# Performance work log

Measured on AMD Instinct MI355X. Metric: run time of the kernel, lower is better.

The kernel has to match this reference:

```python
import jax, jax.numpy as jnp
import numpy as np

L, S, B, E, H, FF = 2048, 2048, 4, 1024, 16, 4096
HD = E // H
EPS = 1e-5


def _ln(x, g, b):
    mu = jnp.mean(x, axis=-1, keepdims=True)
    var = jnp.mean(jnp.square(x - mu), axis=-1, keepdims=True)
    return (x - mu) * jax.lax.rsqrt(var + EPS) * g + b


def _mha(xq, xk, xv, Wq, bq, Wk, bk, Wv, bv, Wo, bo, mask):
    l, bsz, e = xq.shape
    s = xk.shape[0]
    q = (xq @ Wq.T + bq).reshape(l, bsz, H, HD)
    k = (xk @ Wk.T + bk).reshape(s, bsz, H, HD)
    v = (xv @ Wv.T + bv).reshape(s, bsz, H, HD)
    scores = jnp.einsum('lbhd,sbhd->bhls', q, k) / (float(HD) ** 0.5)
    if mask is not None:
        scores = scores + mask  # broadcast (L,S) over (B,H,L,S)
    w = jax.nn.softmax(scores, axis=-1)
    out = jnp.einsum('bhls,sbhd->lbhd', w, v).reshape(l, bsz, e)
    return out @ Wo.T + bo


def setup_inputs() -> dict:
    key = jax.random.key(0)
    ks = jax.random.split(key, 32)
    sc = 0.02
    d = {
        'tgt': jax.random.normal(ks[0], (L, B, E), jnp.float32),
        'memory': jax.random.normal(ks[1], (S, B, E), jnp.float32),
        'tgt_mask': jnp.where(jnp.triu(jnp.ones((L, L), bool), k=1), -jnp.inf, 0.0).astype(jnp.float32),
    }
    def lin(i, out_d, in_d):
        return jax.random.normal(ks[i], (out_d, in_d), jnp.float32) * sc, jnp.zeros((out_d,), jnp.float32)
    for pfx, base in (('sa', 2), ('ca', 6)):
        for j, nm in enumerate(('Wq', 'Wk', 'Wv', 'Wo')):
            W, b = lin(base + j, E, E)
            d[f'{pfx}_{nm}'] = W
            d[f'{pfx}_b{nm[1]}'] = b
    d['W1'], d['b1'] = lin(10, FF, E)
    d['W2'], d['b2'] = lin(11, E, FF)
    for i, nm in enumerate(('ln1', 'ln2', 'ln3')):
        d[f'{nm}_g'] = jnp.ones((E,), jnp.float32)
        d[f'{nm}_b'] = jnp.zeros((E,), jnp.float32)
    return d


def reference(tgt, memory, tgt_mask,
              sa_Wq, sa_bq, sa_Wk, sa_bk, sa_Wv, sa_bv, sa_Wo, sa_bo,
              ca_Wq, ca_bq, ca_Wk, ca_bk, ca_Wv, ca_bv, ca_Wo, ca_bo,
              W1, b1, W2, b2,
              ln1_g, ln1_b, ln2_g, ln2_b, ln3_g, ln3_b):
    # masked self-attention + residual + norm1
    sa = _mha(tgt, tgt, tgt, sa_Wq, sa_bq, sa_Wk, sa_bk, sa_Wv, sa_bv, sa_Wo, sa_bo, tgt_mask)
    x = _ln(tgt + sa, ln1_g, ln1_b)
    # cross-attention + residual + norm2
    ca = _mha(x, memory, memory, ca_Wq, ca_bq, ca_Wk, ca_bk, ca_Wv, ca_bv, ca_Wo, ca_bo, None)
    x = _ln(x + ca, ln2_g, ln2_b)
    # FFN + residual + norm3 (dropout = identity in eval)
    ffn = jax.nn.relu(x @ W1.T + b1) @ W2.T + b2
    return _ln(x + ffn, ln3_g, ln3_b)
```

## Files before the change

kernel.cpp:

```cpp
#include <hip/hip_runtime.h>
#include <cstdint>

typedef unsigned short u16;
typedef __bf16 bf16x8 __attribute__((ext_vector_type(8)));
typedef float f32x4 __attribute__((ext_vector_type(4)));

#define L_ 2048
#define S_ 2048
#define B_ 4
#define E_ 1024
#define H_ 16
#define FF_ 4096
#define M_ (L_*B_)

#define QK_SCALE 0.18033688f

__device__ __forceinline__ unsigned f2bf(float f) {
  unsigned u = __float_as_uint(f);
  return (u + 0x7fffu + ((u >> 16) & 1u)) >> 16;
}
__device__ __forceinline__ float bflo(unsigned u){ return __uint_as_float(u << 16); }
__device__ __forceinline__ float bfhi(unsigned u){ return __uint_as_float(u & 0xffff0000u); }

struct CvtSeg { const float* src; u16* dst; int blk_end; };
struct CvtTab { CvtSeg s[6]; };

__global__ __launch_bounds__(256) void cvt_all(CvtTab t, int nseg) {
  const int blk = blockIdx.x;
  int k = 0;
  while (k < nseg - 1 && blk >= t.s[k].blk_end) k++;
  const int b0 = (k == 0) ? 0 : t.s[k-1].blk_end;
  const int off = (blk - b0) * 1024 + threadIdx.x * 4;
  float4 f = *(const float4*)(t.s[k].src + off);
  uint2 u;
  u.x = f2bf(f.x) | (f2bf(f.y) << 16);
  u.y = f2bf(f.z) | (f2bf(f.w) << 16);
  *(uint2*)(t.s[k].dst + off) = u;
}

struct GTab { u16* o[3]; const float* b[3]; float sc[3]; };

__device__ __forceinline__ void gl_lds16(const u16* g, u16* l) {
  __builtin_amdgcn_global_load_lds(
      (const __attribute__((address_space(1))) unsigned int*)g,
      (__attribute__((address_space(3))) unsigned int*)l, 16, 0, 0);
}

#define RAW_BARRIER() do { \
  asm volatile("" ::: "memory"); \
  __builtin_amdgcn_s_barrier(); \
  asm volatile("" ::: "memory"); \
} while (0)

template<int RELU, int NG>
__global__ __launch_bounds__(512, 2) void gemm256(
    const u16* __restrict__ A,
    const u16* __restrict__ Bw,
    GTab t, int K, int N)
{
  extern __shared__ __align__(16) u16 LDs[];
  const int tid  = threadIdx.x;
  const int lane = tid & 63;
  const int quad = lane >> 4;
  const int l16  = lane & 15;
  const int w    = tid >> 6;
  const int wm   = w >> 2;
  const int wn   = w & 3;
  const int bm = blockIdx.y << 8;
  const int bn = blockIdx.x << 8;

  const int grp = (NG > 1) ? ((int)blockIdx.x >> 2) : 0;
  u16* Cb = t.o[grp];
  const float* bias = t.b[grp];
  const float scale = t.sc[grp];
  const int ld = (NG > 1) ? 1024 : N;

  const int srow = (w << 4) + (lane >> 2);
  const int cg8  = ((lane & 3) ^ ((lane >> 3) & 3)) << 3;
  const u16* pa0 = A  + (size_t)(bm + srow) * K + cg8;
  const u16* pa1 = pa0 + (size_t)128 * K;
  const u16* pb0 = Bw + (size_t)(bn + srow) * K + cg8;
  const u16* pb1 = pb0 + (size_t)128 * K;
  const int wds = w << 9;

  const int swz  = (quad ^ ((l16 >> 1) & 3)) << 3;
  const int aoff = ((wm << 7) + l16) * 32 + swz;
  const int boff = 8192 + ((wn << 6) + l16) * 32 + swz;

  f32x4 acc[8][4];
  #pragma unroll
  for (int i = 0; i < 8; i++)
    #pragma unroll
    for (int j = 0; j < 4; j++)
      acc[i][j] = (f32x4){0.f, 0.f, 0.f, 0.f};

  const int nk = K >> 5;

  #pragma unroll
  for (int kt = 0; kt < 3; kt++) {
    const int sb = kt << 14;
    gl_lds16(pa0 + kt*32, LDs + sb + wds);
    gl_lds16(pa1 + kt*32, LDs + sb + 4096  + wds);
    gl_lds16(pb0 + kt*32, LDs + sb + 8192  + wds);
    gl_lds16(pb1 + kt*32, LDs + sb + 12288 + wds);
  }
  pa0 += 96; pa1 += 96; pb0 += 96; pb1 += 96;
  asm volatile("s_waitcnt vmcnt(8)" ::: "memory");
  RAW_BARRIER();

  for (int it = 0; it < nk; ++it) {
    const int rb = (it & 3) << 14;
    const int sb = ((it + 3) & 3) << 14;

    bf16x8 bfr[4], afr[4];
    #pragma unroll
    for (int nt = 0; nt < 4; nt++)
      bfr[nt] = *(const bf16x8*)(LDs + rb + boff + nt*512);
    #pragma unroll
    for (int mt = 0; mt < 4; mt++)
      afr[mt] = *(const bf16x8*)(LDs + rb + aoff + mt*512);
    gl_lds16(pa0, LDs + sb + wds);
    gl_lds16(pa1, LDs + sb + 4096 + wds);
    RAW_BARRIER();
    __builtin_amdgcn_s_setprio(1);
    #pragma unroll
    for (int mt = 0; mt < 4; mt++)
      #pragma unroll
      for (int nt = 0; nt < 4; nt++)
        acc[mt][nt] = __builtin_amdgcn_mfma_f32_16x16x32_bf16(afr[mt], bfr[nt], acc[mt][nt], 0, 0, 0);
    __builtin_amdgcn_s_setprio(0);
    RAW_BARRIER();

    #pragma unroll
    for (int mt = 0; mt < 4; mt++)
      afr[mt] = *(const bf16x8*)(LDs + rb + aoff + (4 + mt)*512);
    gl_lds16(pb0, LDs + sb + 8192  + wds);
    gl_lds16(pb1, LDs + sb + 12288 + wds);
    asm volatile("s_waitcnt vmcnt(8)" ::: "memory");
    RAW_BARRIER();
    __builtin_amdgcn_s_setprio(1);
    #pragma unroll
    for (int mt = 0; mt < 4; mt++)
      #pragma unroll
      for (int nt = 0; nt < 4; nt++)
        acc[4 + mt][nt] = __builtin_amdgcn_mfma_f32_16x16x32_bf16(afr[mt], bfr[nt], acc[4 + mt][nt], 0, 0, 0);
    __builtin_amdgcn_s_setprio(0);
    RAW_BARRIER();

    if (it + 4 < nk) { pa0 += 32; pa1 += 32; pb0 += 32; pb1 += 32; }
  }

  #pragma unroll
  for (int nt = 0; nt < 4; nt++) {
    const int col = bn + (wn << 6) + nt*16 + l16;
    const int ocol = (NG > 1) ? (col & 1023) : col;
    const float bv = bias[ocol];
    #pragma unroll
    for (int mt = 0; mt < 8; mt++) {
      #pragma unroll
      for (int i = 0; i < 4; i++) {
        const int row = bm + (wm << 7) + mt*16 + quad*4 + i;
        float v = (acc[mt][nt][i] + bv) * scale;
        if (RELU) v = fmaxf(v, 0.0f);
        Cb[(size_t)row * ld + ocol] = (u16)f2bf(v);
      }
    }
  }
}

template<int RELU>
__global__ __launch_bounds__(512, 2) void gemm256n(
    const u16* __restrict__ A,
    const u16* __restrict__ Bw,
    const float* __restrict__ bias,
    u16* __restrict__ C,
    float scale, int K, int N)
{
  extern __shared__ __align__(16) u16 LDs[];
  const int tid  = threadIdx.x;
  const int lane = tid & 63;
  const int quad = lane >> 4;
  const int l16  = lane & 15;
  const int w    = tid >> 6;
  const int wm   = w >> 1;
  const int wn   = w & 1;
  const int bm = blockIdx.y << 8;
  const int bn = blockIdx.x << 7;

  const int srow = (w << 4) + (lane >> 2);
  const int cg8  = ((lane & 3) ^ ((lane >> 3) & 3)) << 3;
  const u16* pa0 = A  + (size_t)(bm + srow) * K + cg8;
  const u16* pa1 = pa0 + (size_t)128 * K;
  const u16* pb0 = Bw + (size_t)(bn + srow) * K + cg8;
  const int wds = w << 9;

  const int swz  = (quad ^ ((l16 >> 1) & 3)) << 3;
  const int aoff = ((wm << 6) + l16) * 32 + swz;
  const int boff = 8192 + ((wn << 6) + l16) * 32 + swz;

  f32x4 acc[4][4];
  #pragma unroll
  for (int i = 0; i < 4; i++)
    #pragma unroll
    for (int j = 0; j < 4; j++)
      acc[i][j] = (f32x4){0.f, 0.f, 0.f, 0.f};

  const int nk = K >> 5;

  #pragma unroll
  for (int kt = 0; kt < 2; kt++) {
    const int sb = kt * 12288;
    gl_lds16(pa0 + kt*32, LDs + sb + wds);
    gl_lds16(pa1 + kt*32, LDs + sb + 4096 + wds);
    gl_lds16(pb0 + kt*32, LDs + sb + 8192 + wds);
  }
  pa0 += 64; pa1 += 64; pb0 += 64;
  asm volatile("s_waitcnt vmcnt(3)" ::: "memory");
  RAW_BARRIER();

  int rb = 0, sb = 24576;
  for (int it = 0; it < nk; ++it) {
    bf16x8 bfr[4], afr0, afr1;
    #pragma unroll
    for (int nt = 0; nt < 4; nt++)
      bfr[nt] = *(const bf16x8*)(LDs + rb + boff + nt*512);
    afr0 = *(const bf16x8*)(LDs + rb + aoff);
    afr1 = *(const bf16x8*)(LDs + rb + aoff + 512);
    gl_lds16(pa0, LDs + sb + wds);
    gl_lds16(pa1, LDs + sb + 4096 + wds);
    RAW_BARRIER();
    __builtin_amdgcn_s_setprio(1);
    #pragma unroll
    for (int nt = 0; nt < 4; nt++) {
      acc[0][nt] = __builtin_amdgcn_mfma_f32_16x16x32_bf16(afr0, bfr[nt], acc[0][nt], 0, 0, 0);
      acc[1][nt] = __builtin_amdgcn_mfma_f32_16x16x32_bf16(afr1, bfr[nt], acc[1][nt], 0, 0, 0);
    }
    __builtin_amdgcn_s_setprio(0);
    RAW_BARRIER();

    afr0 = *(const bf16x8*)(LDs + rb + aoff + 1024);
    afr1 = *(const bf16x8*)(LDs + rb + aoff + 1536);
    gl_lds16(pb0, LDs + sb + 8192 + wds);
    asm volatile("s_waitcnt vmcnt(3)" ::: "memory");
    RAW_BARRIER();
    __builtin_amdgcn_s_setprio(1);
    #pragma unroll
    for (int nt = 0; nt < 4; nt++) {
      acc[2][nt] = __builtin_amdgcn_mfma_f32_16x16x32_bf16(afr0, bfr[nt], acc[2][nt], 0, 0, 0);
      acc[3][nt] = __builtin_amdgcn_mfma_f32_16x16x32_bf16(afr1, bfr[nt], acc[3][nt], 0, 0, 0);
    }
    __builtin_amdgcn_s_setprio(0);
    RAW_BARRIER();

    if (it + 3 < nk) { pa0 += 32; pa1 += 32; pb0 += 32; }
    rb += 12288; if (rb == 36864) rb = 0;
    sb += 12288; if (sb == 36864) sb = 0;
  }

  #pragma unroll
  for (int nt = 0; nt < 4; nt++) {
    const int col = bn + (wn << 6) + nt*16 + l16;
    const float bv = bias[col];
    #pragma unroll
    for (int mt = 0; mt < 4; mt++) {
      #pragma unroll
      for (int i = 0; i < 4; i++) {
        const int row = bm + (wm << 6) + mt*16 + quad*4 + i;
        float v = (acc[mt][nt][i] + bv) * scale;
        if (RELU) v = fmaxf(v, 0.0f);
        C[(size_t)row * N + col] = (u16)f2bf(v);
      }
    }
  }
}

__global__ __launch_bounds__(256) void transpose_v(
    const u16* __restrict__ V, u16* __restrict__ Vt)
{
  const int t = threadIdx.x;
  const int lane = t & 63;
  const int w = t >> 6;
  const int bh = blockIdx.y;
  const int b = bh >> 4, h = bh & 15;
  const int l = (blockIdx.x << 6) + lane;
  const size_t vrow = ((size_t)l * B_ + b) * E_ + h * 64;
  #pragma unroll
  for (int g = 0; g < 2; g++) {
    const int d0 = w * 8 + g * 32;
    uint4 u = *(const uint4*)(V + vrow + d0);
    u16 e[8];
    e[0] = u.x & 0xffff; e[1] = u.x >> 16;
    e[2] = u.y & 0xffff; e[3] = u.y >> 16;
    e[4] = u.z & 0xffff; e[5] = u.z >> 16;
    e[6] = u.w & 0xffff; e[7] = u.w >> 16;
    #pragma unroll
    for (int j = 0; j < 8; j++)
      Vt[(size_t)(bh * 64 + d0 + j) * S_ + l] = e[j];
  }
}

template<int CAUSAL>
__global__ __launch_bounds__(256, 4) void attn_mfma(
    const u16* __restrict__ Q,
    const u16* __restrict__ Kg,
    const u16* __restrict__ Vt,
    u16* __restrict__ O,
    int Skv)
{
  __shared__ __align__(16) u16 Tile[16384];
  const int tid  = threadIdx.x;
  const int lane = tid & 63;
  const int w    = tid >> 6;
  const int l16  = lane & 15;
  const int quad = lane >> 4;
  const int bh = blockIdx.x;
  const int b = bh >> 4, h = bh & 15;
  const int y = blockIdx.y;
  const int q0 = (CAUSAL ? ((y < 8) ? (15 - 2*y) : (2*y - 16)) : y) << 7;
  const int wq = q0 + w*32;

  bf16x8 qf[2][2];
  #pragma unroll
  for (int h2 = 0; h2 < 2; h2++) {
    const size_t qoff = ((size_t)(wq + h2*16 + l16) * B_ + b) * E_ + h*64;
    qf[h2][0] = *(const bf16x8*)(Q + qoff + quad*8);
    qf[h2][1] = *(const bf16x8*)(Q + qoff + 32 + quad*8);
  }

  f32x4 oacc[2][4];
  #pragma unroll
  for (int h2 = 0; h2 < 2; h2++)
    #pragma unroll
    for (int i = 0; i < 4; i++) oacc[h2][i] = (f32x4){0.f,0.f,0.f,0.f};
  float lsum[2] = {0.f, 0.f};

  const int lrow = lane >> 3;
  const int lchunk = (lane & 7) ^ lrow;
  const u16* kp = Kg + ((size_t)(16*w + lrow) * B_ + b) * E_ + h*64 + lchunk*8;
  const u16* vp = Vt + (size_t)(bh*64 + 16*w + lrow) * Skv + lchunk*8;
  const size_t kRow8 = (size_t)8 * B_ * E_;
  const size_t kTile = (size_t)64 * B_ * E_;
  u16* ldsK = Tile + w*1024;
  u16* ldsV = Tile + 4096 + w*1024;

  const int pbase = 8192 + w*2048;
  int aKV[2], aW[4];
  #pragma unroll
  for (int kh = 0; kh < 2; kh++)
    aKV[kh] = l16*64 + (((kh*4 + quad) ^ (l16 & 7)) << 3);
  #pragma unroll
  for (int st = 0; st < 4; st++)
    aW[st] = pbase + l16*64 +
             ((((st*2) + (quad >> 1)) ^ (l16 & 7)) << 3) + ((quad & 1) << 2);

  const int send = CAUSAL ? (q0 + 128) : Skv;
  for (int s0 = 0; s0 < send; s0 += 64) {
    __syncthreads();
    gl_lds16(kp,         ldsK);
    gl_lds16(kp + kRow8, ldsK + 512);
    gl_lds16(vp,         ldsV);
    gl_lds16(vp + 8*Skv, ldsV + 512);
    kp += kTile; vp += 64;
    __syncthreads();

    if (CAUSAL && s0 >= wq + 32) continue;

    f32x4 sacc[2][4];
    #pragma unroll
    for (int h2 = 0; h2 < 2; h2++)
      #pragma unroll
      for (int st = 0; st < 4; st++) sacc[h2][st] = (f32x4){0.f,0.f,0.f,0.f};
    #pragma unroll
    for (int kh = 0; kh < 2; kh++)
      #pragma unroll
      for (int st = 0; st < 4; st++) {
        bf16x8 kf = *(const bf16x8*)(Tile + aKV[kh] + st*1024);
        sacc[0][st] = __builtin_amdgcn_mfma_f32_16x16x32_bf16(kf, qf[0][kh], sacc[0][st], 0, 0, 0);
        sacc[1][st] = __builtin_amdgcn_mfma_f32_16x16x32_bf16(kf, qf[1][kh], sacc[1][st], 0, 0, 0);
      }

    #pragma unroll
    for (int h2 = 0; h2 < 2; h2++) {
      float p[16];
      #pragma unroll
      for (int st = 0; st < 4; st++)
        #pragma unroll
        for (int r = 0; r < 4; r++) p[st*4+r] = sacc[h2][st][r];
      if (CAUSAL && s0 + 63 > wq + h2*16) {
        const int qa = wq + h2*16 + l16;
        #pragma unroll
        for (int st = 0; st < 4; st++)
          #pragma unroll
          for (int r = 0; r < 4; r++)
            if (s0 + st*16 + quad*4 + r > qa) p[st*4+r] = -3e38f;
      }
      #pragma unroll
      for (int i = 0; i < 16; i++) p[i] = exp2f(p[i]);
      float s01 = (p[0]+p[1]) + (p[2]+p[3]);
      float s23 = (p[4]+p[5]) + (p[6]+p[7]);
      float s45 = (p[8]+p[9]) + (p[10]+p[11]);
      float s67 = (p[12]+p[13]) + (p[14]+p[15]);
      lsum[h2] += (s01+s23) + (s45+s67);

      #pragma unroll
      for (int st = 0; st < 4; st++) {
        uint2 d;
        d.x = __builtin_amdgcn_perm(__float_as_uint(p[st*4+1]), __float_as_uint(p[st*4+0]), 0x07060302u);
        d.y = __builtin_amdgcn_perm(__float_as_uint(p[st*4+3]), __float_as_uint(p[st*4+2]), 0x07060302u);
        *(uint2*)(Tile + aW[st] + h2*1024) = d;
      }
    }

    #pragma unroll
    for (int kh = 0; kh < 2; kh++) {
      bf16x8 pf[2];
      #pragma unroll
      for (int h2 = 0; h2 < 2; h2++)
        pf[h2] = *(const bf16x8*)(Tile + pbase + h2*1024 + aKV[kh]);
      #pragma unroll
      for (int dt = 0; dt < 4; dt++) {
        bf16x8 vf = *(const bf16x8*)(Tile + 4096 + aKV[kh] + dt*1024);
        #pragma unroll
        for (int h2 = 0; h2 < 2; h2++)
          oacc[h2][dt] = __builtin_amdgcn_mfma_f32_16x16x32_bf16(pf[h2], vf, oacc[h2][dt], 0, 0, 0);
      }
    }
  }

  #pragma unroll
  for (int h2 = 0; h2 < 2; h2++) {
    float rs = lsum[h2];
    rs += __shfl_xor(rs, 16);
    rs += __shfl_xor(rs, 32);
    const float inv = 1.0f / rs;
    #pragma unroll
    for (int r = 0; r < 4; r++) {
      const float li = __shfl(inv, (quad << 2) + r);
      const int qg = wq + h2*16 + quad*4 + r;
      const size_t orow = ((size_t)qg * B_ + b) * E_ + h*64;
      #pragma unroll
      for (int dt = 0; dt < 4; dt++)
        O[orow + dt*16 + l16] = (u16)f2bf(oacc[h2][dt][r] * li);
    }
  }
}

template<int RF32>
__global__ __launch_bounds__(256) void add_ln(
    const u16* __restrict__ X,
    const float* __restrict__ Rf, const u16* __restrict__ Rb,
    const float* __restrict__ g, const float* __restrict__ be,
    float* __restrict__ outF, u16* __restrict__ outB)
{
  const int row = blockIdx.x;
  const int tid = threadIdx.x;
  const size_t base = (size_t)row * E_;
  uint2 xu = *(const uint2*)(X + base + tid*4);
  float x0 = bflo(xu.x), x1 = bfhi(xu.x), x2 = bflo(xu.y), x3 = bfhi(xu.y);
  float r0, r1, r2, r3;
  if (RF32) {
    float4 rv = *(const float4*)(Rf + base + tid*4);
    r0 = rv.x; r1 = rv.y; r2 = rv.z; r3 = rv.w;
  } else {
    uint2 ru = *(const uint2*)(Rb + base + tid*4);
    r0 = bflo(ru.x); r1 = bfhi(ru.x); r2 = bflo(ru.y); r3 = bfhi(ru.y);
  }
  const float v0 = x0 + r0, v1 = x1 + r1, v2 = x2 + r2, v3 = x3 + r3;
  float s  = v0 + v1 + v2 + v3;
  float s2 = v0*v0 + v1*v1 + v2*v2 + v3*v3;
  #pragma unroll
  for (int off = 32; off >= 1; off >>= 1) {
    s  += __shfl_down(s,  off);
    s2 += __shfl_down(s2, off);
  }
  __shared__ float ps[4], ps2[4];
  const int wv = tid >> 6, lane = tid & 63;
  if (lane == 0) { ps[wv] = s; ps2[wv] = s2; }
  __syncthreads();
  const float ts  = ps[0] + ps[1] + ps[2] + ps[3];
  const float ts2 = ps2[0] + ps2[1] + ps2[2] + ps2[3];
  const float mu  = ts * (1.0f / E_);
  const float var = ts2 * (1.0f / E_) - mu * mu;
  const float rsq = rsqrtf(var + 1e-5f);
  float4 gv = *(const float4*)(g  + tid*4);
  float4 bv = *(const float4*)(be + tid*4);
  const float o0 = (v0 - mu) * rsq * gv.x + bv.x;
  const float o1 = (v1 - mu) * rsq * gv.y + bv.y;
  const float o2 = (v2 - mu) * rsq * gv.z + bv.z;
  const float o3 = (v3 - mu) * rsq * gv.w + bv.w;
  if (outF) {
    float4 ov; ov.x = o0; ov.y = o1; ov.z = o2; ov.w = o3;
    *(float4*)(outF + base + tid*4) = ov;
  }
  if (outB) {
    uint2 u;
    u.x = f2bf(o0) | (f2bf(o1) << 16);
    u.y = f2bf(o2) | (f2bf(o3) << 16);
    *(uint2*)(outB + base + tid*4) = u;
  }
}

extern "C" void kernel_launch(void* const* d_in, const int* in_sizes, int n_in,
                              void* d_out, int out_size, void* d_ws, size_t ws_size,
                              hipStream_t stream) {
  (void)in_sizes; (void)n_in; (void)out_size; (void)ws_size;
  const float* tgt  = (const float*)d_in[0];
  const float* mem  = (const float*)d_in[1];
  const float* saWq = (const float*)d_in[3];  const float* sabq = (const float*)d_in[4];
  const float* saWk = (const float*)d_in[5];  const float* sabk = (const float*)d_in[6];
  const float* saWv = (const float*)d_in[7];  const float* sabv = (const float*)d_in[8];
  const float* saWo = (const float*)d_in[9];  const float* sabo = (const float*)d_in[10];
  const float* caWq = (const float*)d_in[11]; const float* cabq = (const float*)d_in[12];
  const float* caWk = (const float*)d_in[13]; const float* cabk = (const float*)d_in[14];
  const float* caWv = (const float*)d_in[15]; const float* cabv = (const float*)d_in[16];
  const float* caWo = (const float*)d_in[17]; const float* cabo = (const float*)d_in[18];
  const float* W1   = (const float*)d_in[19]; const float* b1   = (const float*)d_in[20];
  const float* W2   = (const float*)d_in[21]; const float* b2   = (const float*)d_in[22];
  const float* ln1g = (const float*)d_in[23]; const float* ln1b = (const float*)d_in[24];
  const float* ln2g = (const float*)d_in[25]; const float* ln2b = (const float*)d_in[26];
  const float* ln3g = (const float*)d_in[27]; const float* ln3b = (const float*)d_in[28];
  float* out = (float*)d_out;

  static bool attr_done = false;
  if (!attr_done) {
    (void)hipFuncSetAttribute(reinterpret_cast<const void*>(&gemm256<0,3>),
                              hipFuncAttributeMaxDynamicSharedMemorySize, 131072);
    (void)hipFuncSetAttribute(reinterpret_cast<const void*>(&gemm256<0,2>),
                              hipFuncAttributeMaxDynamicSharedMemorySize, 131072);
    (void)hipFuncSetAttribute(reinterpret_cast<const void*>(&gemm256<1,1>),
                              hipFuncAttributeMaxDynamicSharedMemorySize, 131072);
    (void)hipFuncSetAttribute(reinterpret_cast<const void*>(&gemm256n<0>),
                              hipFuncAttributeMaxDynamicSharedMemorySize, 73728);
    attr_done = true;
  }

  char* wsp = (char*)d_ws;
  const size_t MB16 = (size_t)16 * 1024 * 1024;
  u16* A  = (u16*)(wsp + 0 * MB16);
  u16* Cq = (u16*)(wsp + 1 * MB16);
  u16* Bm = (u16*)(wsp + 2 * MB16);
  u16* Dk = (u16*)(wsp + 3 * MB16);
  u16* Ev = (u16*)(wsp + 4 * MB16);
  u16* Ff = (u16*)(wsp + 5 * MB16);
  u16* wS = (u16*)(wsp + 6 * MB16);
  u16* hb = Cq;
  const int MEG = 1024 * 1024;

  dim3 blk(256);
  dim3 blk512(512);
  dim3 gN1(8, 32);
  dim3 gQKV256(12, 32);
  dim3 gKV256(8, 32);
  dim3 gFF256(16, 32);
  dim3 ga(B_*H_, L_/128);
  dim3 gt(S_/64, B_*H_);

  {
    CvtTab t{};
    t.s[0] = {tgt,  A,        8192};
    t.s[1] = {mem,  Bm,       16384};
    t.s[2] = {saWq, wS,       17408};
    t.s[3] = {saWk, wS + MEG,   18432};
    t.s[4] = {saWv, wS + 2*MEG, 19456};
    t.s[5] = {saWo, wS + 3*MEG, 20480};
    cvt_all<<<20480, blk, 0, stream>>>(t, 6);
  }

  {
    GTab t{};
    t.o[0]=Cq; t.o[1]=Dk; t.o[2]=Ev;
    t.b[0]=sabq; t.b[1]=sabk; t.b[2]=sabv;
    t.sc[0]=QK_SCALE; t.sc[1]=1.f; t.sc[2]=1.f;
    gemm256<0,3><<<gQKV256, blk512, 131072, stream>>>(A, wS, t, E_, 3*E_);
  }
  transpose_v<<<gt, blk, 0, stream>>>(Ev, Ff);
  attn_mfma<1><<<ga, blk, 0, stream>>>(Cq, Dk, Ff, Cq, S_);
  gemm256n<0><<<gN1, blk512, 73728, stream>>>(Cq, wS + 3*MEG, sabo, Ff, 1.f, E_, E_);
  add_ln<1><<<M_, blk, 0, stream>>>(Ff, tgt, nullptr, ln1g, ln1b, nullptr, A);

  {
    CvtTab t{};
    t.s[0] = {caWq, wS,        1024};
    t.s[1] = {caWk, wS + MEG,    2048};
    t.s[2] = {caWv, wS + 2*MEG,  3072};
    t.s[3] = {caWo, wS + 3*MEG,  4096};
    cvt_all<<<4096, blk, 0, stream>>>(t, 4);
  }

  gemm256n<0><<<gN1, blk512, 73728, stream>>>(A, wS, cabq, Cq, QK_SCALE, E_, E_);
  {
    GTab t{};
    t.o[0]=Dk; t.o[1]=Ev; t.o[2]=Ev;
    t.b[0]=cabk; t.b[1]=cabv; t.b[2]=cabv;
    t.sc[0]=1.f; t.sc[1]=1.f; t.sc[2]=1.f;
    gemm256<0,2><<<gKV256, blk512, 131072, stream>>>(Bm, wS + MEG, t, E_, 2*E_);
  }
  transpose_v<<<gt, blk, 0, stream>>>(Ev, Ff);
  attn_mfma<0><<<ga, blk, 0, stream>>>(Cq, Dk, Ff, Cq, S_);
  gemm256n<0><<<gN1, blk512, 73728, stream>>>(Cq, wS + 3*MEG, cabo, Ff, 1.f, E_, E_);
  add_ln<0><<<M_, blk, 0, stream>>>(Ff, nullptr, A, ln2g, ln2b, nullptr, A);

  {
    CvtTab t{};
    t.s[0] = {W1, wS, 4096};
    cvt_all<<<4096, blk, 0, stream>>>(t, 1);
  }
  {
    GTab t{};
    t.o[0]=hb; t.o[1]=hb; t.o[2]=hb;
    t.b[0]=b1; t.b[1]=b1; t.b[2]=b1;
    t.sc[0]=1.f; t.sc[1]=1.f; t.sc[2]=1.f;
    gemm256<1,1><<<gFF256, blk512, 131072, stream>>>(A, wS, t, E_, FF_);
  }
  {
    CvtTab t{};
    t.s[0] = {W2, wS, 4096};
    cvt_all<<<4096, blk, 0, stream>>>(t, 1);
  }
  gemm256n<0><<<gN1, blk512, 73728, stream>>>(hb, wS, b2, Ff, 1.f, FF_, E_);
  add_ln<0><<<M_, blk, 0, stream>>>(Ff, nullptr, A, ln3g, ln3b, out, nullptr);
}
```

Baseline: 810.4 us.

## Compute softmax row sums via MFMA with ones and tile V transpose through LDS

The attention kernel drops the per-lane scalar sums of the exponentiated scores and the shuffle reduction. Instead it accumulates row sums with an extra MFMA per step, multiplying the bf16 probability fragments by a vector of ones, so the sums use the same bf16-rounded values as the P·V product. The V transpose kernel now stages a 64x64 tile in padded shared memory, so both the loads and the stores to global memory are 16-byte vectors instead of scattered 2-byte writes. The cost is extra MFMA work in the inner loop and a block-level barrier in the transpose.

```diff
diff --git a/kernel.cpp b/kernel.cpp
--- a/kernel.cpp
+++ b/kernel.cpp
@@ -277,25 +277,41 @@
 __global__ __launch_bounds__(256) void transpose_v(
     const u16* __restrict__ V, u16* __restrict__ Vt)
 {
-  const int t = threadIdx.x;
-  const int lane = t & 63;
-  const int w = t >> 6;
+  __shared__ unsigned T32[64][36];
+  const int t  = threadIdx.x;
   const int bh = blockIdx.y;
   const int b = bh >> 4, h = bh & 15;
-  const int l = (blockIdx.x << 6) + lane;
-  const size_t vrow = ((size_t)l * B_ + b) * E_ + h * 64;
-  #pragma unroll
-  for (int g = 0; g < 2; g++) {
-    const int d0 = w * 8 + g * 32;
-    uint4 u = *(const uint4*)(V + vrow + d0);
-    u16 e[8];
-    e[0] = u.x & 0xffff; e[1] = u.x >> 16;
-    e[2] = u.y & 0xffff; e[3] = u.y >> 16;
-    e[4] = u.z & 0xffff; e[5] = u.z >> 16;
-    e[6] = u.w & 0xffff; e[7] = u.w >> 16;
-    #pragma unroll
-    for (int j = 0; j < 8; j++)
-      Vt[(size_t)(bh * 64 + d0 + j) * S_ + l] = e[j];
+  const int lblk = blockIdx.x << 6;
+
+  {
+    const int il = t >> 2;
+    const int c  = (t & 3) << 4;
+    const u16* src = V + ((size_t)(lblk + il) * B_ + b) * E_ + h*64 + c;
+    uint4 u0 = *(const uint4*)src;
+    uint4 u1 = *(const uint4*)(src + 8);
+    *(uint4*)&T32[il][(c >> 1)]     = u0;
+    *(uint4*)&T32[il][(c >> 1) + 4] = u1;
+  }
+  __syncthreads();
+
+  {
+    const int d  = t >> 2;
+    const int ls = (t & 3) << 4;
+    const int dp = d >> 1, hi = d & 1;
+    unsigned o[16];
+    #pragma unroll
+    for (int j = 0; j < 16; j++) {
+      unsigned w = T32[ls + j][dp];
+      o[j] = hi ? (w >> 16) : (w & 0xffffu);
+    }
+    uint4 v0, v1;
+    v0.x = o[0]  | (o[1]  << 16); v0.y = o[2]  | (o[3]  << 16);
+    v0.z = o[4]  | (o[5]  << 16); v0.w = o[6]  | (o[7]  << 16);
+    v1.x = o[8]  | (o[9]  << 16); v1.y = o[10] | (o[11] << 16);
+    v1.z = o[12] | (o[13] << 16); v1.w = o[14] | (o[15] << 16);
+    u16* dst = Vt + (size_t)(bh*64 + d) * S_ + lblk + ls;
+    *(uint4*)dst       = v0;
+    *(uint4*)(dst + 8) = v1;
   }
 }
 
@@ -327,12 +343,17 @@
     qf[h2][1] = *(const bf16x8*)(Q + qoff + 32 + quad*8);
   }
 
+  const uint4 ones_u = {0x3F803F80u, 0x3F803F80u, 0x3F803F80u, 0x3F803F80u};
+  const bf16x8 ones = *(const bf16x8*)&ones_u;
+
   f32x4 oacc[2][4];
   #pragma unroll
   for (int h2 = 0; h2 < 2; h2++)
     #pragma unroll
     for (int i = 0; i < 4; i++) oacc[h2][i] = (f32x4){0.f,0.f,0.f,0.f};
-  float lsum[2] = {0.f, 0.f};
+  f32x4 lsacc[2];
+  lsacc[0] = (f32x4){0.f,0.f,0.f,0.f};
+  lsacc[1] = (f32x4){0.f,0.f,0.f,0.f};
 
   const int lrow = lane >> 3;
   const int lchunk = (lane & 7) ^ lrow;
@@ -396,11 +417,6 @@
       }
       #pragma unroll
       for (int i = 0; i < 16; i++) p[i] = exp2f(p[i]);
-      float s01 = (p[0]+p[1]) + (p[2]+p[3]);
-      float s23 = (p[4]+p[5]) + (p[6]+p[7]);
-      float s45 = (p[8]+p[9]) + (p[10]+p[11]);
-      float s67 = (p[12]+p[13]) + (p[14]+p[15]);
-      lsum[h2] += (s01+s23) + (s45+s67);
 
       #pragma unroll
       for (int st = 0; st < 4; st++) {
@@ -417,6 +433,8 @@
       #pragma unroll
       for (int h2 = 0; h2 < 2; h2++)
         pf[h2] = *(const bf16x8*)(Tile + pbase + h2*1024 + aKV[kh]);
+      lsacc[0] = __builtin_amdgcn_mfma_f32_16x16x32_bf16(pf[0], ones, lsacc[0], 0, 0, 0);
+      lsacc[1] = __builtin_amdgcn_mfma_f32_16x16x32_bf16(pf[1], ones, lsacc[1], 0, 0, 0);
       #pragma unroll
       for (int dt = 0; dt < 4; dt++) {
         bf16x8 vf = *(const bf16x8*)(Tile + 4096 + aKV[kh] + dt*1024);
@@ -429,18 +447,14 @@
 
   #pragma unroll
   for (int h2 = 0; h2 < 2; h2++) {
-    float rs = lsum[h2];
-    rs += __shfl_xor(rs, 16);
-    rs += __shfl_xor(rs, 32);
-    const float inv = 1.0f / rs;
     #pragma unroll
     for (int r = 0; r < 4; r++) {
-      const float li = __shfl(inv, (quad << 2) + r);
+      const float inv = 1.0f / lsacc[h2][r];
       const int qg = wq + h2*16 + quad*4 + r;
       const size_t orow = ((size_t)qg * B_ + b) * E_ + h*64;
       #pragma unroll
       for (int dt = 0; dt < 4; dt++)
-        O[orow + dt*16 + l16] = (u16)f2bf(oacc[h2][dt][r] * li);
+        O[orow + dt*16 + l16] = (u16)f2bf(oacc[h2][dt][r] * inv);
     }
   }
 }
```

Result: no change. 810.7 us (+0.0%).
